# Kernel optimization log

Measured on AMD Instinct MI355X. Metric: run time of the kernel, lower is better.

## Reference

```python
import jax, jax.numpy as jnp
from jax import lax
import numpy as np

B, CB, HW, HID, P, NC = 128, 200, 32, 32, 4, 10
DEPTH, D, DI, DS, DR, K = 4, 128, 256, 16, 8, 4
G = HW // P                  # 8 -> 64 spatial patches
SPA_N = G * G
SPE_N = CB // 2              # 100 spectral patches
HS, HE = HW // 2 - 5 // 2, HW // 2 + 5 // 2 + 1   # centered 5x5 spectral crop: 14:19


def _sincos_1d(d, pos):
    omega = 1.0 / 10000 ** (np.arange(d // 2, dtype=np.float64) / (d / 2.0))
    out = np.outer(pos.reshape(-1).astype(np.float64), omega)
    return np.concatenate([np.sin(out), np.cos(out)], axis=1)


def _spa_pos_embed():
    # MAE get_2d_sincos_pos_embed with cls_token=True (zeros row FIRST)
    gw, gh = np.meshgrid(np.arange(G, dtype=np.float64), np.arange(G, dtype=np.float64))
    emb = np.concatenate([_sincos_1d(D // 2, gw), _sincos_1d(D // 2, gh)], axis=1)
    return np.concatenate([np.zeros((1, D)), emb], axis=0)  # (SPA_N+1, D)


def _spe_pos_embed():
    pe = np.zeros((SPE_N + 1, D))
    pos = np.arange(SPE_N + 1, dtype=np.float64)[:, None]
    div = np.exp(np.arange(0, D, 2) * -(np.log(10000.0) / D))
    pe[:, 0::2] = np.sin(pos * div)
    pe[:, 1::2] = np.cos(pos * div)
    return pe


def setup_inputs():
    keys = iter(jax.random.split(jax.random.key(0), 64))
    r = lambda shape, s=0.02: jax.random.normal(next(keys), shape, jnp.float32) * s
    return dict(
        x=jax.random.normal(next(keys), (B, CB, HW, HW), jnp.float32),
        spa_pos=jnp.asarray(_spa_pos_embed(), jnp.float32),
        spe_pos=jnp.asarray(_spe_pos_embed(), jnp.float32),
        dr_w1=r((HID, CB)), dr_b1=r((HID,)), bn1_g=1.0 + r((HID,)), bn1_b=r((HID,)),
        dr_w2=r((HID, HID)), dr_b2=r((HID,)), bn2_g=1.0 + r((HID,)), bn2_b=r((HID,)),
        spa_pw=r((D, HID, P, P)), spa_pb=r((D,)),
        spe_pw=r((D, 25, 2)), spe_pb=r((D,)),
        spa_cls=r((1, 1, D)), spe_cls=r((1, 1, D)),
        ln_g=jnp.ones((DEPTH, 2, D), jnp.float32), ln_b=jnp.zeros((DEPTH, 2, D), jnp.float32),
        in_w=r((DEPTH, 2, 2 * DI, D)),
        conv_w=r((DEPTH, 2, DI, K), 0.2), conv_b=r((DEPTH, 2, DI)),
        xp_w=r((DEPTH, 2, DR + 2 * DS, DI)),
        dtp_w=r((DEPTH, 2, DI, DR), 0.1), dtp_b=r((DEPTH, 2, DI), 0.1),
        a_log=jnp.log(jnp.tile(jnp.arange(1.0, DS + 1.0, dtype=jnp.float32), (DEPTH, 2, DI, 1))),
        d_p=jnp.ones((DEPTH, 2, DI), jnp.float32),
        out_w=r((DEPTH, 2, D, DI)),
        l1_w=r((DEPTH, D, D)),
        head_w=r((NC, D)), head_b=r((NC,)),
    )


def _layernorm(x, g, b, eps=1e-6):
    m = x.mean(-1, keepdims=True)
    v = jnp.mean((x - m) ** 2, axis=-1, keepdims=True)
    return (x - m) * lax.rsqrt(v + eps) * g + b


def _batchnorm(x, g, b, eps=1e-5):
    # training-mode BN: biased batch stats over (B,H,W) per channel
    m = x.mean((0, 2, 3), keepdims=True)
    v = x.var((0, 2, 3), keepdims=True)
    return (x - m) * lax.rsqrt(v + eps) * g[None, :, None, None] + b[None, :, None, None]


def _ssm(x, in_w, cw, cb, xpw, dtw, dtb, alog, dpar, ow):
    # standard Mamba selective-scan block (expand=2, d_conv=4)
    Bb, L, _ = x.shape
    xz = jnp.einsum('bld,ed->ble', x, in_w)
    xc, z = jnp.split(xz, 2, axis=-1)
    xt = jnp.pad(xc.transpose(0, 2, 1), ((0, 0), (0, 0), (K - 1, 0)))  # causal pad
    xt = lax.conv_general_dilated(xt, cw[:, None, :], (1,), 'VALID', feature_group_count=DI)
    xc = jax.nn.silu(xt + cb[None, :, None]).transpose(0, 2, 1)        # (B,L,DI)
    dbl = jnp.einsum('bld,ed->ble', xc, xpw)
    dt = jax.nn.softplus(jnp.einsum('blr,dr->bld', dbl[..., :DR], dtw) + dtb)
    Bm, Cm = dbl[..., DR:DR + DS], dbl[..., DR + DS:]
    dA = jnp.exp(dt[..., None] * (-jnp.exp(alog)))                     # (B,L,DI,DS)
    dBx = (dt * xc)[..., None] * Bm[:, :, None, :]                     # (B,L,DI,DS)

    def step(h, ab):
        h = ab[0] * h + ab[1]
        return h, h

    _, hs = lax.scan(step, jnp.zeros((Bb, DI, DS), xc.dtype),
                     (dA.transpose(1, 0, 2, 3), dBx.transpose(1, 0, 2, 3)))
    y = jnp.einsum('lbds,bls->bld', hs, Cm) + xc * dpar
    return jnp.einsum('bld,ed->ble', y * jax.nn.silu(z), ow)


def _block(inp, lg, lb, sp):
    # block_1D: bidirectional SSM with trailing cls token kept in place
    xn = _layernorm(inp, lg, lb)
    x1 = _ssm(xn, *sp)
    x2 = jnp.concatenate([xn[:, :-1][:, ::-1], xn[:, -1:]], axis=1)
    x3 = _ssm(x2, *sp)
    x3 = jnp.concatenate([x3[:, :-1][:, ::-1], x3[:, -1:]], axis=1)
    return (x1 + x3) * 0.5 + inp


def reference(x, spa_pos, spe_pos, dr_w1, dr_b1, bn1_g, bn1_b, dr_w2, dr_b2, bn2_g, bn2_b,
              spa_pw, spa_pb, spe_pw, spe_pb, spa_cls, spe_cls, ln_g, ln_b, in_w, conv_w,
              conv_b, xp_w, dtp_w, dtp_b, a_log, d_p, out_w, l1_w, head_w, head_b):
    Bb = x.shape[0]
    # dimen_redu: 1x1 conv -> BN -> ReLU -> 1x1 conv -> BN
    h = jnp.einsum('bchw,oc->bohw', x, dr_w1) + dr_b1[None, :, None, None]
    h = jax.nn.relu(_batchnorm(h, bn1_g, bn1_b))
    h = jnp.einsum('bchw,oc->bohw', h, dr_w2) + dr_b2[None, :, None, None]
    h = _batchnorm(h, bn2_g, bn2_b)
    # spatial patch embed (conv k=stride=P == patchify + matmul)
    hr = h.reshape(Bb, HID, G, P, G, P)
    x_spa = jnp.einsum('bcipjq,dcpq->bijd', hr, spa_pw).reshape(Bb, SPA_N, D) + spa_pb
    x_spa = x_spa + spa_pos[None, :-1, :]
    x_spa = jnp.concatenate([x_spa, jnp.broadcast_to(spa_cls + spa_pos[None, -1:, :], (Bb, 1, D))], axis=1)
    # spectral patch embed on centered 5x5 crop: Conv1d(25->D, k=stride=2) over bands
    xc = x[:, :, HS:HE, HS:HE].reshape(Bb, CB, 25).transpose(0, 2, 1).reshape(Bb, 25, SPE_N, 2)
    x_spe = jnp.einsum('bcls,dcs->bld', xc, spe_pw) + spe_pb
    x_spe = x_spe + spe_pos[None, :-1, :]
    x_spe = jnp.concatenate([x_spe, jnp.broadcast_to(spe_cls + spe_pos[None, -1:, :], (Bb, 1, D))], axis=1)
    for i in range(DEPTH):
        spa_p = (in_w[i, 0], conv_w[i, 0], conv_b[i, 0], xp_w[i, 0], dtp_w[i, 0], dtp_b[i, 0], a_log[i, 0], d_p[i, 0], out_w[i, 0])
        spe_p = (in_w[i, 1], conv_w[i, 1], conv_b[i, 1], xp_w[i, 1], dtp_w[i, 1], dtp_b[i, 1], a_log[i, 1], d_p[i, 1], out_w[i, 1])
        x_spa = _block(x_spa, ln_g[i, 0], ln_b[i, 0], spa_p)
        x_spe = _block(x_spe, ln_g[i, 1], ln_b[i, 1], spe_p)
        # sigmoid-gated fusion (fu=True)
        c = (x_spa[:, (x_spa.shape[1] - 1) // 2, :] + x_spe.mean(axis=1)) * 0.5
        sig = jax.nn.sigmoid(c @ l1_w[i].T)[:, None, :]
        x_spa = x_spa * sig
        x_spe = x_spe * sig
    out = (x_spa[:, -1] + x_spe[:, -1]) * 0.5   # cls tokens (global_pool=False)
    return out @ head_w.T + head_b
```

## Files before the change

### kernel.cpp

```cpp
#include <hip/hip_runtime.h>
#include <math.h>

typedef float4 f4;
typedef __attribute__((ext_vector_type(8))) short short8v;
typedef __attribute__((ext_vector_type(4))) float f32x4;

constexpr int B_ = 128, CB_ = 200, HW_ = 32, HID_ = 32, D_ = 128, DI_ = 256;
constexpr int DS_ = 16, DR_ = 8, KC_ = 4, DEPTH_ = 4, NC_ = 10;
constexpr int LSPA_ = 65, LSPE_ = 101, NPIX_ = 1024;
constexpr int M1_ = B_ * NPIX_;
constexpr int NSPA4 = B_*LSPA_*D_/4;
constexpr int NSPE4 = B_*LSPE_*D_/4;
constexpr int NW_ = DEPTH_*2*512*D_;

constexpr size_t O_XSPA = 0;
constexpr size_t O_XSPE = O_XSPA + (size_t)B_*LSPA_*D_;
constexpr size_t O_SC   = O_XSPE + (size_t)B_*LSPE_*D_;
constexpr size_t O_BN1P = O_SC + 512;
constexpr size_t O_BN2P = O_BN1P + 512*64;
constexpr size_t O_U    = O_BN2P + 512*64;
constexpr size_t O_HP1  = O_U;
constexpr size_t O_HP2  = O_U + (size_t)M1_*HID_;
constexpr size_t O_WTR  = O_HP2 + (size_t)M1_*HID_;
constexpr size_t O_XZSPA = O_U;
constexpr size_t O_XZSPE = O_XZSPA + (size_t)B_*LSPA_*512;
constexpr size_t O_XCSPA = O_XZSPE + (size_t)B_*LSPE_*512;
constexpr size_t O_XCSPE = O_XCSPA + (size_t)2*B_*LSPA_*DI_;
constexpr size_t O_DBSPA = O_XCSPE + (size_t)2*B_*LSPE_*DI_;
constexpr size_t O_DBSPE = O_DBSPA + (size_t)2*B_*LSPA_*40;
constexpr size_t O_YZSPA = O_DBSPE + (size_t)2*B_*LSPE_*40;
constexpr size_t O_YZSPE = O_YZSPA + (size_t)2*B_*LSPA_*DI_;
constexpr size_t O_WHI  = O_YZSPE + (size_t)2*B_*LSPE_*DI_;
constexpr size_t O_WLO  = O_WHI + NW_/2;

static __device__ __forceinline__ unsigned short f2bf(float f) {
    unsigned int u = __float_as_uint(f);
    unsigned int r = u + 0x7fffu + ((u >> 16) & 1u);
    return (unsigned short)(r >> 16);
}
static __device__ __forceinline__ float bf2f(unsigned short h) {
    return __uint_as_float(((unsigned int)h) << 16);
}

__global__ __launch_bounds__(256) void k_stem1(const float* __restrict__ x,
        const float* __restrict__ w1, const float* __restrict__ b1,
        float* __restrict__ hpre1, float* __restrict__ part)
{
    __shared__ float smem[8448];
    float* sw = smem;
    const int t = threadIdx.x;
    for (int i = t; i < CB_*HID_; i += 256) {
        int c = i >> 5, o = i & 31;
        sw[i] = w1[o*CB_ + c];
    }
    const int m = blockIdx.x*256 + t;
    const int b = m >> 10, pix = m & 1023;
    const float* xp = x + (size_t)b*CB_*NPIX_ + pix;
    float h[HID_];
    #pragma unroll
    for (int o = 0; o < HID_; o++) h[o] = b1[o];
    __syncthreads();
    for (int c8 = 0; c8 < CB_; c8 += 8) {
        float xv[8];
        #pragma unroll
        for (int j = 0; j < 8; j++) xv[j] = xp[(size_t)(c8 + j)*NPIX_];
        #pragma unroll
        for (int j = 0; j < 8; j++) {
            const f4* wr = (const f4*)(sw + (c8 + j)*HID_);
            #pragma unroll
            for (int o8 = 0; o8 < 8; o8++) {
                f4 wv = wr[o8];
                h[o8*4+0] = fmaf(xv[j], wv.x, h[o8*4+0]);
                h[o8*4+1] = fmaf(xv[j], wv.y, h[o8*4+1]);
                h[o8*4+2] = fmaf(xv[j], wv.z, h[o8*4+2]);
                h[o8*4+3] = fmaf(xv[j], wv.w, h[o8*4+3]);
            }
        }
    }
    f4* hp = (f4*)(hpre1 + (size_t)m*HID_);
    #pragma unroll
    for (int o = 0; o < HID_; o += 4) { f4 v = {h[o],h[o+1],h[o+2],h[o+3]}; hp[o>>2] = v; }
    __syncthreads();
    float* sred = smem;
    #pragma unroll
    for (int o = 0; o < HID_; o++) sred[t*33 + o] = h[o];
    __syncthreads();
    if (t < HID_) {
        float s = 0.f, q = 0.f;
        for (int j = 0; j < 256; j++) { float v = sred[j*33 + t]; s += v; q += v*v; }
        part[blockIdx.x*64 + t]      = s;
        part[blockIdx.x*64 + 32 + t] = q;
    }
}

__global__ void k_bnfix(const float* __restrict__ part, const float* __restrict__ g,
        const float* __restrict__ bta, float* __restrict__ scale, float* __restrict__ shift)
{
    const int o = threadIdx.x;
    if (o >= 32) return;
    float s = 0.f, q = 0.f;
    for (int j = 0; j < 512; j++) { s += part[j*64 + o]; q += part[j*64 + 32 + o]; }
    const float mean = s / (float)M1_;
    const float var  = q / (float)M1_ - mean*mean;
    const float sc = g[o] * rsqrtf(var + 1e-5f);
    scale[o] = sc;
    shift[o] = bta[o] - mean*sc;
}

__global__ void k_bnfix_spa(const float* __restrict__ part, const float* __restrict__ g,
        const float* __restrict__ bta, const float* __restrict__ spa_pw,
        const float* __restrict__ spa_pb, float* __restrict__ scale,
        float* __restrict__ shift, float* __restrict__ spa_shift)
{
    __shared__ float ssh[32];
    const int t = threadIdx.x;
    if (t < 32) {
// ... 1 lines not shown
        for (int j = 0; j < 512; j++) { s += part[j*64 + t]; q += part[j*64 + 32 + t]; }
        const float mean = s / (float)M1_;
        const float var  = q / (float)M1_ - mean*mean;
        const float sc = g[t] * rsqrtf(var + 1e-5f);
        scale[t] = sc;
        const float sh = bta[t] - mean*sc;
        shift[t] = sh;
        ssh[t] = sh;
    }
    __syncthreads();
    float acc = spa_pb[t];
    for (int c = 0; c < HID_; c++) {
        float wsum = 0.f;
        #pragma unroll
        for (int pq = 0; pq < 16; pq++) wsum += spa_pw[((size_t)t*HID_ + c)*16 + pq];
        acc = fmaf(ssh[c], wsum, acc);
    }
    spa_shift[t] = acc;
}

__global__ __launch_bounds__(256) void k_stem2(const float* __restrict__ hpre1,
        const float* __restrict__ w2, const float* __restrict__ b2,
        const float* __restrict__ sc1, const float* __restrict__ sh1,
        float* __restrict__ hpre2, float* __restrict__ part)
{
    __shared__ float smem[8448];
    __shared__ float s_sc[HID_], s_sh[HID_], s_b2[HID_];
    float* sw = smem;
    const int t = threadIdx.x;
    for (int i = t; i < HID_*HID_; i += 256) {
        int c = i >> 5, o = i & 31;
        sw[i] = w2[o*HID_ + c];
    }
    if (t < HID_) { s_sc[t] = sc1[t]; s_sh[t] = sh1[t]; s_b2[t] = b2[t]; }
    __syncthreads();
    const int m = blockIdx.x*256 + t;
    const f4* hp = (const f4*)(hpre1 + (size_t)m*HID_);
    float a[HID_];
    #pragma unroll
    for (int c = 0; c < HID_; c += 4) { f4 v = hp[c>>2]; a[c]=v.x; a[c+1]=v.y; a[c+2]=v.z; a[c+3]=v.w; }
    #pragma unroll
    for (int c = 0; c < HID_; c++) a[c] = fmaxf(fmaf(a[c], s_sc[c], s_sh[c]), 0.f);
    float h[HID_];
    #pragma unroll
    for (int o = 0; o < HID_; o++) h[o] = s_b2[o];
    #pragma unroll
    for (int c = 0; c < HID_; c++) {
        const f4* wr = (const f4*)(sw + c*HID_);
        #pragma unroll
        for (int o8 = 0; o8 < 8; o8++) {
            f4 wv = wr[o8];
            h[o8*4+0] = fmaf(a[c], wv.x, h[o8*4+0]);
            h[o8*4+1] = fmaf(a[c], wv.y, h[o8*4+1]);
            h[o8*4+2] = fmaf(a[c], wv.z, h[o8*4+2]);
            h[o8*4+3] = fmaf(a[c], wv.w, h[o8*4+3]);
        }
    }
    f4* op = (f4*)(hpre2 + (size_t)m*HID_);
    #pragma unroll
    for (int o = 0; o < HID_; o += 4) { f4 v = {h[o],h[o+1],h[o+2],h[o+3]}; op[o>>2] = v; }
    __syncthreads();
    float* sred = smem;
    #pragma unroll
    for (int o = 0; o < HID_; o++) sred[t*33 + o] = h[o];
    __syncthreads();
    if (t < HID_) {
        float s = 0.f, q = 0.f;
        for (int j = 0; j < 256; j++) { float v = sred[j*33 + t]; s += v; q += v*v; }
        part[blockIdx.x*64 + t]      = s;
        part[blockIdx.x*64 + 32 + t] = q;
    }
}

__global__ __launch_bounds__(256) void k_wtr(const float* __restrict__ spa_pw,
        float* __restrict__ wtr)
{
    const int idx = blockIdx.x*256 + threadIdx.x;
    if (idx >= 65536) return;
    const int pq = idx >> 12, dc = idx & 4095;
    wtr[idx] = spa_pw[dc*16 + pq];
}

__global__ __launch_bounds__(256) void k_wsplit(const float* __restrict__ in_w,
        unsigned short* __restrict__ whi, unsigned short* __restrict__ wlo)
{
    const int i = blockIdx.x*256 + threadIdx.x;
    if (i >= NW_) return;
    const float f = in_w[i];
    const unsigned short h = f2bf(f);
    whi[i] = h;
    wlo[i] = f2bf(f - bf2f(h));
}

__global__ __launch_bounds__(256) void k_patch(const float* __restrict__ hpre2,
        const float* __restrict__ wtr, const float* __restrict__ sc2,
        const float* __restrict__ spa_shift, const float* __restrict__ spa_pos,
        const float* __restrict__ spa_cls, float* __restrict__ xspa)
{
    const int b = blockIdx.x >> 1, half = blockIdx.x & 1;
    const int n0 = half*32;
    __shared__ __align__(16) float sA[32*36];
    __shared__ __align__(16) float sB[128*36];
    __shared__ float s_sc[HID_];
    const int t = threadIdx.x;
    if (t < HID_) s_sc[t] = sc2[t];
    const int ty = t >> 4, tx = t & 15;
    float acc[2][8];
    #pragma unroll
    for (int i = 0; i < 2; i++)
        #pragma unroll
        for (int j = 0; j < 8; j++) acc[i][j] = 0.f;
    for (int pq = 0; pq < 16; pq++) {
        const int p = pq >> 2, q = pq & 3;
        __syncthreads();
        for (int idx = t; idx < 32*8; idx += 256) {
            const int n = idx >> 3, c4 = (idx & 7)*4;
            const int nn = n0 + n;
            const int ii = nn >> 3, jj = nn & 7;
            const int pix = (ii*4 + p)*HW_ + jj*4 + q;
            f4 v = *(const f4*)(hpre2 + ((size_t)b*NPIX_ + pix)*HID_ + c4);
            float* pp = &sA[n*36 + c4];
            pp[0] = v.x*s_sc[c4]; pp[1] = v.y*s_sc[c4+1]; pp[2] = v.z*s_sc[c4+2]; pp[3] = v.w*s_sc[c4+3];
        }
        for (int idx = t; idx < 128*8; idx += 256) {
            const int dd = idx >> 3, c4 = (idx & 7)*4;
            f4 v = *(const f4*)(wtr + pq*4096 + dd*HID_ + c4);
            float* pp = &sB[dd*36 + c4];
            pp[0]=v.x; pp[1]=v.y; pp[2]=v.z; pp[3]=v.w;
        }
        __syncthreads();
        #pragma unroll
        for (int kq = 0; kq < 8; kq++) {
            f4 a0 = *(const f4*)&sA[(ty*2+0)*36 + kq*4];
            f4 a1 = *(const f4*)&sA[(ty*2+1)*36 + kq*4];
            #pragma unroll
            for (int j = 0; j < 8; j++) {
                const f4 bv = *(const f4*)&sB[(tx + 16*j)*36 + kq*4];
                acc[0][j] = fmaf(a0.x,bv.x,fmaf(a0.y,bv.y,fmaf(a0.z,bv.z,fmaf(a0.w,bv.w,acc[0][j]))));
                acc[1][j] = fmaf(a1.x,bv.x,fmaf(a1.y,bv.y,fmaf(a1.z,bv.z,fmaf(a1.w,bv.w,acc[1][j]))));
            }
        }
    }
    #pragma unroll
    for (int i = 0; i < 2; i++) {
        const int n = n0 + ty*2 + i;
        float* orow = xspa + ((size_t)b*LSPA_ + n)*D_;
        #pragma unroll
        for (int j = 0; j < 8; j++) {
            const int d = tx + 16*j;
            orow[d] = acc[i][j] + spa_shift[d] + spa_pos[n*D_ + d];
        }
    }
    if (half == 0 && t < D_)
        xspa[((size_t)b*LSPA_ + 64)*D_ + t] = spa_cls[t] + spa_pos[64*D_ + t];
}

__global__ __launch_bounds__(256) void k_spe(const float* __restrict__ x,
        const float* __restrict__ spe_pw, const float* __restrict__ spe_pb,
        const float* __restrict__ spe_pos, const float* __restrict__ spe_cls,
        float* __restrict__ xspe)
{
    const int b = blockIdx.x >> 1, half = blockIdx.x & 1;
    __shared__ float sx[100*25];
    __shared__ float sw[D_*51];
    const int t = threadIdx.x;
    for (int idx = t; idx < 100*25; idx += 256) {
        const int ch = idx / 25 + half*100, c = idx % 25;
        sx[idx] = x[(size_t)b*CB_*NPIX_ + (size_t)ch*NPIX_ + (14 + c/5)*HW_ + 14 + c%5];
    }
    for (int idx = t; idx < D_*50; idx += 256) sw[(idx/50)*51 + idx%50] = spe_pw[idx];
    __syncthreads();
    const int d = t & 127, ls = t >> 7;
    for (int j = ls; j < 50; j += 2) {
        const int l = half*50 + j;
// ... 97 lines not shown
            dh[0] = h0; dh[1] = h1;
            dl[0] = l0; dl[1] = l1;
        }
        __syncthreads();
        short8v ah[2], al[2], bh[4], bl[4];
        #pragma unroll
        for (int i = 0; i < 2; i++) {
            const int ro = (wm*32 + i*16 + lr)*136 + kc*32 + lg*8;
            ah[i] = *(const short8v*)&sAhi[ro];
            al[i] = *(const short8v*)&sAlo[ro];
        }
        #pragma unroll
        for (int j = 0; j < 4; j++) {
            const int co = (wn*64 + j*16 + lr)*40 + lg*8;
            bh[j] = *(const short8v*)&sBhi[co];
            bl[j] = *(const short8v*)&sBlo[co];
        }
        #pragma unroll
        for (int i = 0; i < 2; i++)
            #pragma unroll
            for (int j = 0; j < 4; j++) {
                acc[i][j] = __builtin_amdgcn_mfma_f32_16x16x32_bf16(ah[i], bh[j], acc[i][j], 0, 0, 0);
                acc[i][j] = __builtin_amdgcn_mfma_f32_16x16x32_bf16(ah[i], bl[j], acc[i][j], 0, 0, 0);
                acc[i][j] = __builtin_amdgcn_mfma_f32_16x16x32_bf16(al[i], bh[j], acc[i][j], 0, 0, 0);
            }
        __syncthreads();
    }

    #pragma unroll
    for (int i = 0; i < 2; i++) {
        const int rbase = m0 + wm*32 + i*16 + lg*4;
        #pragma unroll
        for (int j = 0; j < 4; j++) {
            const int col = n0 + wn*64 + j*16 + lr;
            #pragma unroll
            for (int r = 0; r < 4; r++)
                XZ[(size_t)(rbase + r)*512 + col] = acc[i][j][r];
        }
    }
}

__global__ __launch_bounds__(256) void k_conv(const float* __restrict__ xz_spa,
        const float* __restrict__ xz_spe, float* __restrict__ xc_spa, float* __restrict__ xc_spe,
        const float* __restrict__ conv_w, const float* __restrict__ conv_b, int depth)
{
    const int br = blockIdx.z;
    const int L = br ? LSPE_ : LSPA_;
    const int nt = (L + 15) / 16;
    const int b = blockIdx.x % B_;
    const int tl = blockIdx.x / B_;
    if (tl >= nt) return;
    const int l0 = tl * 16;
    const int d = threadIdx.x;
    const float* XZ = (br ? xz_spe : xz_spa) + (size_t)b*L*512 + d;
    float* XC0 = (br ? xc_spe : xc_spa) + ((size_t)(0*B_ + b)*L)*DI_ + d;
    float* XC1 = (br ? xc_spe : xc_spa) + ((size_t)(1*B_ + b)*L)*DI_ + d;
    const size_t w = (size_t)depth*2 + br;
    const float* cw = conv_w + (w*DI_ + d)*KC_;
    const float cb = conv_b[w*DI_ + d];
    const float w0 = cw[0], w1 = cw[1], w2 = cw[2], w3 = cw[3];
    float av[19], ev[19];
    #pragma unroll
    for (int j = 0; j < 19; j++) {
        const int l = l0 - 3 + j;
        const bool ok = (l >= 0) && (l < L);
        av[j] = ok ? XZ[(size_t)l*512] : 0.f;
        const int lr = (l == L-1) ? (L-1) : (L-2-l);
        ev[j] = ok ? XZ[(size_t)lr*512] : 0.f;
    }
    #pragma unroll
    for (int c = 0; c < 16; c++) {
        const int l = l0 + c;
        if (l < L) {
            float acc0 = fmaf(av[c],w0, fmaf(av[c+1],w1, fmaf(av[c+2],w2, fmaf(av[c+3],w3, cb))));
            float acc1 = fmaf(ev[c],w0, fmaf(ev[c+1],w1, fmaf(ev[c+2],w2, fmaf(ev[c+3],w3, cb))));
            XC0[(size_t)l*DI_] = acc0 / (1.f + __expf(-acc0));
            XC1[(size_t)l*DI_] = acc1 / (1.f + __expf(-acc1));
        }
    }
}

__global__ __launch_bounds__(256) void k_xp(const float* __restrict__ xc_spa,
        const float* __restrict__ xc_spe, float* __restrict__ dbl_spa, float* __restrict__ dbl_spe,
        const float* __restrict__ xp_w, int depth)
{
    const int br = blockIdx.z;
    const int L = br ? LSPE_ : LSPA_;
    const int M2 = 2*B_*L;
    const int tile = blockIdx.x;
    if (tile*64 >= M2) return;
    const float* XC = br ? xc_spe : xc_spa;
    float* DBL = br ? dbl_spe : dbl_spa;
    const float* W = xp_w + ((size_t)depth*2 + br)*40*DI_;
    __shared__ __align__(16) float sA[64*68];
    __shared__ __align__(16) float sB[40*68];
    const int t = threadIdx.x;
    const int m0 = tile*64;
    const int ty = t >> 2, tx = t & 3;
    float acc[10];
    #pragma unroll
    for (int j = 0; j < 10; j++) acc[j] = 0.f;
    for (int kc = 0; kc < 4; kc++) {
        __syncthreads();
        for (int idx = t; idx < 64*16; idx += 256) {
            const int r = idx >> 4, k4 = (idx & 15)*4;
            f4 v = *(const f4*)(XC + ((size_t)(m0 + r))*DI_ + kc*64 + k4);
            float* p = &sA[r*68 + k4];
            p[0]=v.x; p[1]=v.y; p[2]=v.z; p[3]=v.w;
        }
        for (int idx = t; idx < 40*16; idx += 256) {
            const int n = idx >> 4, k4 = (idx & 15)*4;
            f4 v = *(const f4*)(W + (size_t)n*DI_ + kc*64 + k4);
            float* p = &sB[n*68 + k4];
            p[0]=v.x; p[1]=v.y; p[2]=v.z; p[3]=v.w;
        }
        __syncthreads();
        #pragma unroll
        for (int kq = 0; kq < 16; kq++) {
            const f4 a = *(const f4*)&sA[ty*68 + kq*4];
            #pragma unroll
            for (int j = 0; j < 10; j++) {
                const f4 bv = *(const f4*)&sB[(tx*10 + j)*68 + kq*4];
                acc[j] = fmaf(a.x,bv.x,fmaf(a.y,bv.y,fmaf(a.z,bv.z,fmaf(a.w,bv.w,acc[j]))));
            }
        }
    }
    float* outp = DBL + (size_t)(m0 + ty)*40 + tx*10;
    #pragma unroll
    for (int j = 0; j < 10; j++) outp[j] = acc[j];
}

__global__ __launch_bounds__(256) void k_scan(
        const float* __restrict__ xz_spa, const float* __restrict__ xz_spe,
        const float* __restrict__ xc_spa, const float* __restrict__ xc_spe,
        const float* __restrict__ dbl_spa, const float* __restrict__ dbl_spe,
        float* __restrict__ yz_spa, float* __restrict__ yz_spe,
        const float* __restrict__ a_log, const float* __restrict__ dtp_w,
        const float* __restrict__ dtp_b, const float* __restrict__ d_p, int depth)
{
    const int br = blockIdx.z, dir = blockIdx.y;
    const int L = br ? LSPE_ : LSPA_;
    const int b = blockIdx.x;
    const int t = threadIdx.x;
    const float* XZ   = (br ? xz_spe : xz_spa) + (size_t)b*L*512;
    const float* XC   = (br ? xc_spe : xc_spa) + ((size_t)(dir*B_ + b))*L*DI_;
    const float* DBLp = (br ? dbl_spe : dbl_spa) + ((size_t)(dir*B_ + b))*L*40;
    float* YZ = (br ? yz_spe : yz_spa) + ((size_t)(dir*B_ + b))*L*DI_;
    const size_t w = (size_t)depth*2 + br;
    const float nA0 = -__expf(a_log[((size_t)(w*DI_ + t))*DS_]) * 1.4426950408889634f;
    float dtw[8];
    #pragma unroll
    for (int r = 0; r < 8; r++) dtw[r] = dtp_w[((size_t)(w*DI_ + t))*DR_ + r];
    const float dtb = dtp_b[w*DI_ + t];
    const float dpv = d_p[w*DI_ + t];
    float h[16];
    #pragma unroll
    for (int u = 0; u < 16; u++) h[u] = 0.f;

    __shared__ __align__(16) float sD[2][320];
    float rd0, rd1;
    float rxA[8], rzA[8], rxB[8], rzB[8];

#define LOADD(J0) do {                                                        \
    const int lim_ = ((L - (J0) < 8) ? (L - (J0)) : 8) * 40;                  \
    rd0 = (t < lim_) ? DBLp[(size_t)(J0)*40 + t] : 0.f;                       \
    rd1 = (t + 256 < lim_) ? DBLp[(size_t)(J0)*40 + t + 256] : 0.f;           \
} while(0)

#define WRITED(BUF) do {                                                      \
    sD[BUF][t] = rd0;                                                         \
    if (t < 64) sD[BUF][t + 256] = rd1;                                       \
} while(0)

#define LOADX(J0, RX, RZ) do {                                                \
    _Pragma("unroll")                                                         \
    for (int j_ = 0; j_ < 8; ++j_) {                                          \
        const int row_ = (J0) + j_;                                           \
        if (row_ < L) {                                                       \
            RX[j_] = XC[(size_t)row_*DI_ + t];                                \
            const int zr_ = dir ? ((row_ == L-1) ? (L-1) : (L-2-row_)) : row_;\
            RZ[j_] = XZ[(size_t)zr_*512 + 256 + t];                           \
        } else { RX[j_] = 0.f; RZ[j_] = 0.f; }                                \
    }                                                                         \
} while(0)

#define SCAN_CHUNK(J0, BUF, RX, RZ) do {                                      \
    _Pragma("unroll")                                                         \
    for (int c_ = 0; c_ < 8; ++c_) {                                          \
        const int l_ = (J0) + c_;                                             \
        if (l_ < L) {                                                         \
            const float* dr = &sD[BUF][c_*40];                                \
            const f4 q0 = *(const f4*)(dr);                                   \
            const f4 q1 = *(const f4*)(dr + 4);                               \
            float raw = dtb;                                                  \
            raw = fmaf(q0.x,dtw[0],raw); raw = fmaf(q0.y,dtw[1],raw);         \
            raw = fmaf(q0.z,dtw[2],raw); raw = fmaf(q0.w,dtw[3],raw);         \
            raw = fmaf(q1.x,dtw[4],raw); raw = fmaf(q1.y,dtw[5],raw);         \
            raw = fmaf(q1.z,dtw[6],raw); raw = fmaf(q1.w,dtw[7],raw);         \
            const float er = __builtin_amdgcn_exp2f(raw * 1.4426950408889634f);\
            const float dt = (raw > 20.f) ? raw                               \
                : __log2f(1.f + er) * 0.6931471805599453f;                    \
            const float xcv = RX[c_], zv = RZ[c_];                            \
            const float c2 = dt * xcv;                                        \
            const float E1 = __builtin_amdgcn_exp2f(nA0 * dt);                \
            const float E2 = E1 * E1;                                         \
            const f4 B0=*(const f4*)(dr+8),  B1=*(const f4*)(dr+12);          \
            const f4 B2=*(const f4*)(dr+16), B3=*(const f4*)(dr+20);          \
            const f4 C0=*(const f4*)(dr+24), C1=*(const f4*)(dr+28);          \
            const f4 C2=*(const f4*)(dr+32), C3=*(const f4*)(dr+36);          \
            float eo = E1, ee = E2, y = 0.f;                                  \
            h[0]=fmaf(h[0],eo,c2*B0.x);  y=fmaf(h[0],C0.x,y);                 \
            h[1]=fmaf(h[1],ee,c2*B0.y);  y=fmaf(h[1],C0.y,y);                 \
            eo*=E2; h[2]=fmaf(h[2],eo,c2*B0.z);  y=fmaf(h[2],C0.z,y);         \
            ee*=E2; h[3]=fmaf(h[3],ee,c2*B0.w);  y=fmaf(h[3],C0.w,y);         \
            eo*=E2; h[4]=fmaf(h[4],eo,c2*B1.x);  y=fmaf(h[4],C1.x,y);         \
            ee*=E2; h[5]=fmaf(h[5],ee,c2*B1.y);  y=fmaf(h[5],C1.y,y);         \
            eo*=E2; h[6]=fmaf(h[6],eo,c2*B1.z);  y=fmaf(h[6],C1.z,y);         \
            ee*=E2; h[7]=fmaf(h[7],ee,c2*B1.w);  y=fmaf(h[7],C1.w,y);         \
            eo*=E2; h[8]=fmaf(h[8],eo,c2*B2.x);  y=fmaf(h[8],C2.x,y);         \
            ee*=E2; h[9]=fmaf(h[9],ee,c2*B2.y);  y=fmaf(h[9],C2.y,y);         \
            eo*=E2; h[10]=fmaf(h[10],eo,c2*B2.z); y=fmaf(h[10],C2.z,y);       \
            ee*=E2; h[11]=fmaf(h[11],ee,c2*B2.w); y=fmaf(h[11],C2.w,y);       \
            eo*=E2; h[12]=fmaf(h[12],eo,c2*B3.x); y=fmaf(h[12],C3.x,y);       \
            ee*=E2; h[13]=fmaf(h[13],ee,c2*B3.y); y=fmaf(h[13],C3.y,y);       \
            eo*=E2; h[14]=fmaf(h[14],eo,c2*B3.z); y=fmaf(h[14],C3.z,y);       \
            ee*=E2; h[15]=fmaf(h[15],ee,c2*B3.w); y=fmaf(h[15],C3.w,y);       \
            const float yt = fmaf(xcv, dpv, y);                               \
            const float sg = __builtin_amdgcn_rcpf(                           \
                1.f + __builtin_amdgcn_exp2f(-zv * 1.4426950408889634f));     \
            const int ls_ = dir ? ((l_ == L-1) ? (L-1) : (L-2-l_)) : l_;      \
            YZ[(size_t)ls_*DI_ + t] = yt * (zv * sg);                         \
        }                                                                     \
    }                                                                         \
} while(0)

    const int nch = (L + 7) >> 3;
    LOADD(0);
    LOADX(0, rxA, rzA);
    WRITED(0);
    __syncthreads();
    int ck = 0;
    while (true) {
        {
            const int j0 = ck*8;
            const bool more = (ck + 1 < nch);
            if (more) { LOADD(j0 + 8); LOADX(j0 + 8, rxB, rzB); }
            SCAN_CHUNK(j0, 0, rxA, rzA);
            if (more) WRITED(1);
            __syncthreads();
            if (!more) break;
            ck++;
        }
        {
            const int j0 = ck*8;
            const bool more = (ck + 1 < nch);
            if (more) { LOADD(j0 + 8); LOADX(j0 + 8, rxA, rzA); }
            SCAN_CHUNK(j0, 1, rxB, rzB);
            if (more) WRITED(0);
            __syncthreads();
            if (!more) break;
            ck++;
        }
    }
#undef LOADD
#undef WRITED
#undef LOADX
#undef SCAN_CHUNK
}

__global__ __launch_bounds__(256) void k_out(float* __restrict__ xspa, float* __restrict__ xspe,
        const float* __restrict__ yz_spa, const float* __restrict__ yz_spe,
        const float* __restrict__ out_w, int depth)
{
    const int br = blockIdx.z;
    const int L = br ? LSPE_ : LSPA_;
    const int M = B_ * L;
    const int tile = blockIdx.x;
    if (tile*32 >= M) return;
    float* X = br ? xspe : xspa;
    const float* Y0 = br ? yz_spe : yz_spa;
    const float* Y1 = Y0 + (size_t)B_*L*DI_;
    const float* W = out_w + ((size_t)depth*2 + br)*D_*DI_;
    __shared__ __align__(16) float sA[32*68];
    __shared__ __align__(16) float sB[128*68];
    const int t = threadIdx.x;
    const int m0 = tile*32;
    const int ty = t >> 4, tx = t & 15;
    float acc[2][8];
    #pragma unroll
    for (int i = 0; i < 2; i++)
        #pragma unroll
        for (int j = 0; j < 8; j++) acc[i][j] = 0.f;
    for (int kc = 0; kc < 4; kc++) {
        __syncthreads();
        for (int idx = t; idx < 32*16; idx += 256) {
            const int r = idx >> 4, k4 = (idx & 15)*4;
            const size_t go = ((size_t)(m0 + r))*DI_ + kc*64 + k4;
            f4 v0 = *(const f4*)(Y0 + go);
            f4 v1 = *(const f4*)(Y1 + go);
            float* p = &sA[r*68 + k4];
            p[0]=v0.x+v1.x; p[1]=v0.y+v1.y; p[2]=v0.z+v1.z; p[3]=v0.w+v1.w;
        }
        for (int idx = t; idx < 128*64; idx += 256) {
            const int n = idx >> 6, kk = idx & 63;
            sB[n*68 + kk] = W[(size_t)n*DI_ + kc*64 + kk];
        }
        __syncthreads();
        #pragma unroll
        for (int kq = 0; kq < 16; kq++) {
            f4 a0 = *(const f4*)&sA[(ty*2+0)*68 + kq*4];
            f4 a1 = *(const f4*)&sA[(ty*2+1)*68 + kq*4];
            #pragma unroll
            for (int j = 0; j < 8; j++) {
                const f4 bv = *(const f4*)&sB[(tx + 16*j)*68 + kq*4];
                acc[0][j] = fmaf(a0.x,bv.x,fmaf(a0.y,bv.y,fmaf(a0.z,bv.z,fmaf(a0.w,bv.w,acc[0][j]))));
                acc[1][j] = fmaf(a1.x,bv.x,fmaf(a1.y,bv.y,fmaf(a1.z,bv.z,fmaf(a1.w,bv.w,acc[1][j]))));
            }
        }
    }
    #pragma unroll
    for (int i = 0; i < 2; i++) {
        float* orow = X + (size_t)(m0 + ty*2 + i)*D_;
        #pragma unroll
        for (int j = 0; j < 8; j++) {
            const int n = tx + 16*j;
            orow[n] += 0.5f*acc[i][j];
        }
    }
}

__global__ __launch_bounds__(256) void k_gate1(const float* __restrict__ xspa,
        const float* __restrict__ xspe, const float* __restrict__ l1_w,
        float* __restrict__ sig, int depth)
{
    __shared__ float sp[2][128];
    __shared__ float sc[128];
    __shared__ float sduo[256];
    const int b = blockIdx.x, t = threadIdx.x;
    const int dd = t & 127, rh = t >> 7;
    float s = 0.f;
    for (int l = rh; l < LSPE_; l += 2) s += xspe[((size_t)b*LSPE_ + l)*D_ + dd];
    sp[rh][dd] = s;
    __syncthreads();
    if (t < 128)
        sc[t] = 0.5f*(xspa[((size_t)b*LSPA_ + 32)*D_ + t] + (sp[0][t]+sp[1][t])*(1.f/101.f));
    __syncthreads();
    {
        const float* wr = l1_w + (size_t)depth*D_*D_ + (size_t)dd*D_ + rh*64;
        float acc = 0.f;
        #pragma unroll 4
        for (int k = 0; k < 64; k++) acc = fmaf(sc[rh*64 + k], wr[k], acc);
        sduo[t] = acc;
    }
    __syncthreads();
    if (t < 128)
        sig[(size_t)b*D_ + t] = 1.f/(1.f + __expf(-(sduo[t] + sduo[t+128])));
}

__global__ __launch_bounds__(256) void k_gate2(float* __restrict__ xspa,
        float* __restrict__ xspe, const float* __restrict__ sig)
{
    const int fi = blockIdx.x*256 + threadIdx.x;
    f4* base;
    int b, pos;
    if (fi < NSPA4) {
        base = (f4*)xspa + fi;
        b = fi / (LSPA_*32);
        pos = fi & 31;
    } else {
        const int j = fi - NSPA4;
        if (j >= NSPE4) return;
        base = (f4*)xspe + j;
        b = j / (LSPE_*32);
        pos = j & 31;
    }
    const f4 sg = *((const f4*)sig + b*32 + pos);
    f4 v = *base;
    v.x *= sg.x; v.y *= sg.y; v.z *= sg.z; v.w *= sg.w;
    *base = v;
}

__global__ void k_head(const float* __restrict__ xspa, const float* __restrict__ xspe,
        const float* __restrict__ head_w, const float* __restrict__ head_b, float* __restrict__ out)
{
    __shared__ float sv[D_];
    const int b = blockIdx.x, t = threadIdx.x;
    if (t < D_) sv[t] = 0.5f*(xspa[((size_t)b*LSPA_ + 64)*D_ + t] + xspe[((size_t)b*LSPE_ + 100)*D_ + t]);
    __syncthreads();
    if (t < NC_) {
        float acc = head_b[t];
        for (int k = 0; k < D_; k++) acc = fmaf(sv[k], head_w[t*D_ + k], acc);
        out[b*NC_ + t] = acc;
    }
}

extern "C" void kernel_launch(void* const* d_in, const int* in_sizes, int n_in,
                              void* d_out, int out_size, void* d_ws, size_t ws_size,
                              hipStream_t stream)
{
    const float* x       = (const float*)d_in[0];
    const float* spa_pos = (const float*)d_in[1];
    const float* spe_pos = (const float*)d_in[2];
    const float* dr_w1   = (const float*)d_in[3];
    const float* dr_b1   = (const float*)d_in[4];
    const float* bn1_g   = (const float*)d_in[5];
    const float* bn1_b   = (const float*)d_in[6];
    const float* dr_w2   = (const float*)d_in[7];
    const float* dr_b2   = (const float*)d_in[8];
    const float* bn2_g   = (const float*)d_in[9];
    const float* bn2_b   = (const float*)d_in[10];
    const float* spa_pw  = (const float*)d_in[11];
    const float* spa_pb  = (const float*)d_in[12];
    const float* spe_pw  = (const float*)d_in[13];
    const float* spe_pb  = (const float*)d_in[14];
    const float* spa_cls = (const float*)d_in[15];
    const float* spe_cls = (const float*)d_in[16];
    const float* ln_g    = (const float*)d_in[17];
    const float* ln_b    = (const float*)d_in[18];
    const float* in_w    = (const float*)d_in[19];
    const float* conv_w  = (const float*)d_in[20];
    const float* conv_b  = (const float*)d_in[21];
    const float* xp_w    = (const float*)d_in[22];
    const float* dtp_w   = (const float*)d_in[23];
    const float* dtp_b   = (const float*)d_in[24];
    const float* a_log   = (const float*)d_in[25];
    const float* d_p     = (const float*)d_in[26];
    const float* out_w   = (const float*)d_in[27];
    const float* l1_w    = (const float*)d_in[28];
    const float* head_w  = (const float*)d_in[29];
    const float* head_b  = (const float*)d_in[30];

    float* ws = (float*)d_ws;
    float* xspa   = ws + O_XSPA;
    float* xspe   = ws + O_XSPE;
    float* scale1 = ws + O_SC;
    float* shift1 = ws + O_SC + 32;
    float* scale2 = ws + O_SC + 64;
    float* shift2 = ws + O_SC + 96;
    float* spa_sh = ws + O_SC + 128;
    float* bn1p   = ws + O_BN1P;
    float* bn2p   = ws + O_BN2P;
    float* sig    = ws + O_BN1P;
    float* hpre1  = ws + O_HP1;
    float* hpre2  = ws + O_HP2;
    float* wtr    = ws + O_WTR;
    float* xz_spa = ws + O_XZSPA;
    float* xz_spe = ws + O_XZSPE;
    float* xc_spa = ws + O_XCSPA;
    float* xc_spe = ws + O_XCSPE;
    float* db_spa = ws + O_DBSPA;
    float* db_spe = ws + O_DBSPE;
    float* yz_spa = ws + O_YZSPA;
    float* yz_spe = ws + O_YZSPE;
    unsigned short* whi = (unsigned short*)(ws + O_WHI);
    unsigned short* wlo = (unsigned short*)(ws + O_WLO);

    hipLaunchKernelGGL(k_stem1, dim3(512), dim3(256), 0, stream, x, dr_w1, dr_b1, hpre1, bn1p);
    hipLaunchKernelGGL(k_bnfix, dim3(1), dim3(32), 0, stream, bn1p, bn1_g, bn1_b, scale1, shift1);
    hipLaunchKernelGGL(k_wtr, dim3(256), dim3(256), 0, stream, spa_pw, wtr);
    hipLaunchKernelGGL(k_wsplit, dim3(NW_/256), dim3(256), 0, stream, in_w, whi, wlo);
    hipLaunchKernelGGL(k_stem2, dim3(512), dim3(256), 0, stream, hpre1, dr_w2, dr_b2, scale1, shift1, hpre2, bn2p);
    hipLaunchKernelGGL(k_bnfix_spa, dim3(1), dim3(128), 0, stream, bn2p, bn2_g, bn2_b,
                       spa_pw, spa_pb, scale2, shift2, spa_sh);
    hipLaunchKernelGGL(k_patch, dim3(256), dim3(256), 0, stream, hpre2, wtr, scale2, spa_sh, spa_pos, spa_cls, xspa);
    hipLaunchKernelGGL(k_spe, dim3(256), dim3(256), 0, stream, x, spe_pw, spe_pb, spe_pos, spe_cls, xspe);

    for (int i = 0; i < DEPTH_; i++) {
        hipLaunchKernelGGL(k_ln_in, dim3(202, 4, 2), dim3(256), 0, stream,
                           xspa, xspe, xz_spa, xz_spe, whi, wlo, ln_g, ln_b, i);
        hipLaunchKernelGGL(k_conv, dim3(B_*7, 1, 2), dim3(256), 0, stream,
                           xz_spa, xz_spe, xc_spa, xc_spe, conv_w, conv_b, i);
        hipLaunchKernelGGL(k_xp, dim3(404, 1, 2), dim3(256), 0, stream,
                           xc_spa, xc_spe, db_spa, db_spe, xp_w, i);
        hipLaunchKernelGGL(k_scan, dim3(B_, 2, 2), dim3(256), 0, stream,
                           xz_spa, xz_spe, xc_spa, xc_spe, db_spa, db_spe,
                           yz_spa, yz_spe, a_log, dtp_w, dtp_b, d_p, i);
        hipLaunchKernelGGL(k_out, dim3(404, 1, 2), dim3(256), 0, stream,
                           xspa, xspe, yz_spa, yz_spe, out_w, i);
        hipLaunchKernelGGL(k_gate1, dim3(128), dim3(256), 0, stream, xspa, xspe, l1_w, sig, i);
        hipLaunchKernelGGL(k_gate2, dim3((NSPA4 + NSPE4 + 255)/256), dim3(256), 0, stream,
                           xspa, xspe, sig);
    }
    hipLaunchKernelGGL(k_head, dim3(128), dim3(128), 0, stream,
                       xspa, xspe, head_w, head_b, (float*)d_out);
}
```

Before: 868.4 us.

## Port x_proj and out_proj GEMMs to split-bf16 MFMA with pre-split weights

Rewrites the x_proj and out_proj GEMM kernels to use bf16 MFMA 16x16x32 instructions instead of scalar FP32 FMAs. Each operand is split into a bf16 high part and a bf16 residual, and three MFMAs per tile pair keep near-FP32 accuracy. Weights are pre-split once in the extended k_wsplit kernel, while activations are split on the fly as they are staged into shared memory. Tile sizes double, which halves the grid. The cost is extra conversion work, more shared memory, and wasted MFMA columns, since x_proj's 40 output columns are padded to 48.

```diff
diff --git a/kernel.cpp b/kernel.cpp
--- a/kernel.cpp
+++ b/kernel.cpp
@@ -11,7 +11,9 @@
 constexpr int M1_ = B_ * NPIX_;
 constexpr int NSPA4 = B_*LSPA_*D_/4;
 constexpr int NSPE4 = B_*LSPE_*D_/4;
-constexpr int NW_ = DEPTH_*2*512*D_;
+constexpr int NWI_ = DEPTH_*2*512*D_;
+constexpr int NWO_ = DEPTH_*2*D_*DI_;
+constexpr int NWX_ = DEPTH_*2*40*DI_;
 
 constexpr size_t O_XSPA = 0;
 constexpr size_t O_XSPE = O_XSPA + (size_t)B_*LSPA_*D_;
@@ -30,8 +32,12 @@
 constexpr size_t O_DBSPE = O_DBSPA + (size_t)2*B_*LSPA_*40;
 constexpr size_t O_YZSPA = O_DBSPE + (size_t)2*B_*LSPE_*40;
 constexpr size_t O_YZSPE = O_YZSPA + (size_t)2*B_*LSPA_*DI_;
-constexpr size_t O_WHI  = O_YZSPE + (size_t)2*B_*LSPE_*DI_;
-constexpr size_t O_WLO  = O_WHI + NW_/2;
+constexpr size_t O_WHI_I = O_YZSPE + (size_t)2*B_*LSPE_*DI_;
+constexpr size_t O_WLO_I = O_WHI_I + NWI_/2;
+constexpr size_t O_WHI_O = O_WLO_I + NWI_/2;
+constexpr size_t O_WLO_O = O_WHI_O + NWO_/2;
+constexpr size_t O_WHI_X = O_WLO_O + NWO_/2;
+constexpr size_t O_WLO_X = O_WHI_X + NWX_/2;
 
 static __device__ __forceinline__ unsigned short f2bf(float f) {
     unsigned int u = __float_as_uint(f);
@@ -199,14 +205,20 @@
 }
 
 __global__ __launch_bounds__(256) void k_wsplit(const float* __restrict__ in_w,
-        unsigned short* __restrict__ whi, unsigned short* __restrict__ wlo)
+        const float* __restrict__ out_w, const float* __restrict__ xp_w,
+        unsigned short* __restrict__ whiI, unsigned short* __restrict__ wloI,
+        unsigned short* __restrict__ whiO, unsigned short* __restrict__ wloO,
+        unsigned short* __restrict__ whiX, unsigned short* __restrict__ wloX)
 {
     const int i = blockIdx.x*256 + threadIdx.x;
-    if (i >= NW_) return;
-    const float f = in_w[i];
+    float f; unsigned short* ph; unsigned short* pl; int j;
+    if (i < NWI_) { j = i; f = in_w[j]; ph = whiI; pl = wloI; }
+    else if (i < NWI_ + NWO_) { j = i - NWI_; f = out_w[j]; ph = whiO; pl = wloO; }
+    else if (i < NWI_ + NWO_ + NWX_) { j = i - NWI_ - NWO_; f = xp_w[j]; ph = whiX; pl = wloX; }
+    else return;
     const unsigned short h = f2bf(f);
-    whi[i] = h;
-    wlo[i] = f2bf(f - bf2f(h));
+    ph[j] = h;
+    pl[j] = f2bf(f - bf2f(h));
 }
 
 __global__ __launch_bounds__(256) void k_patch(const float* __restrict__ hpre2,
@@ -470,52 +482,106 @@
 
 __global__ __launch_bounds__(256) void k_xp(const float* __restrict__ xc_spa,
         const float* __restrict__ xc_spe, float* __restrict__ dbl_spa, float* __restrict__ dbl_spe,
-        const float* __restrict__ xp_w, int depth)
+        const unsigned short* __restrict__ whiX, const unsigned short* __restrict__ wloX, int depth)
 {
     const int br = blockIdx.z;
     const int L = br ? LSPE_ : LSPA_;
     const int M2 = 2*B_*L;
-    const int tile = blockIdx.x;
-    if (tile*64 >= M2) return;
+    const int m0 = blockIdx.x*128;
+    if (m0 >= M2) return;
     const float* XC = br ? xc_spe : xc_spa;
     float* DBL = br ? dbl_spe : dbl_spa;
-    const float* W = xp_w + ((size_t)depth*2 + br)*40*DI_;
-    __shared__ __align__(16) float sA[64*68];
-    __shared__ __align__(16) float sB[40*68];
+    const size_t wb = ((size_t)depth*2 + br) * 40 * (size_t)DI_;
+    const unsigned short* WH = whiX + wb;
+    const unsigned short* WL = wloX + wb;
+
+    __shared__ __align__(16) unsigned short sAhi[128*40];
+    __shared__ __align__(16) unsigned short sAlo[128*40];
+    __shared__ __align__(16) unsigned short sBhi[48*40];
+    __shared__ __align__(16) unsigned short sBlo[48*40];
+
     const int t = threadIdx.x;
-    const int m0 = tile*64;
-    const int ty = t >> 2, tx = t & 3;
-    float acc[10];
-    #pragma unroll
-    for (int j = 0; j < 10; j++) acc[j] = 0.f;
-    for (int kc = 0; kc < 4; kc++) {
+    const int wv = t >> 6, l = t & 63;
+    const int lr = l & 15, lg = l >> 4;
+    f32x4 acc[2][3];
+    #pragma unroll
+    for (int i = 0; i < 2; i++)
+        #pragma unroll
+        for (int j = 0; j < 3; j++) acc[i][j] = (f32x4){0.f,0.f,0.f,0.f};
+
+    for (int kc = 0; kc < 8; kc++) {
+        {
+            const int r = t >> 1, off = (t & 1)*16;
+            const float* src = XC + (size_t)(m0 + r)*DI_ + kc*32 + off;
+            unsigned short uh[16], ul[16];
+            #pragma unroll
+            for (int j4 = 0; j4 < 4; j4++) {
+                f4 u = *(const f4*)(src + j4*4);
+                float vv[4] = {u.x, u.y, u.z, u.w};
+                #pragma unroll
+                for (int e = 0; e < 4; e++) {
+                    const unsigned short h = f2bf(vv[e]);
+                    uh[j4*4+e] = h;
+                    ul[j4*4+e] = f2bf(vv[e] - bf2f(h));
+                }
+            }
+            #pragma unroll
+            for (int j4 = 0; j4 < 4; j4++) {
+                ushort4 a = {uh[j4*4], uh[j4*4+1], uh[j4*4+2], uh[j4*4+3]};
+                ushort4 b = {ul[j4*4], ul[j4*4+1], ul[j4*4+2], ul[j4*4+3]};
+                *(ushort4*)&sAhi[r*40 + off + j4*4] = a;
+                *(ushort4*)&sAlo[r*40 + off + j4*4] = b;
+            }
+            if (t < 192) {
+                const int n = t >> 2, q = t & 3;
+                uint4 h0 = {0,0,0,0}, l0 = {0,0,0,0};
+                if (n < 40) {
+                    const size_t g = (size_t)n*DI_ + kc*32 + q*8;
+                    h0 = *(const uint4*)(WH + g);
+                    l0 = *(const uint4*)(WL + g);
+                }
+                *(uint4*)&sBhi[n*40 + q*8] = h0;
+                *(uint4*)&sBlo[n*40 + q*8] = l0;
+            }
+        }
         __syncthreads();
-        for (int idx = t; idx < 64*16; idx += 256) {
-            const int r = idx >> 4, k4 = (idx & 15)*4;
-            f4 v = *(const f4*)(XC + ((size_t)(m0 + r))*DI_ + kc*64 + k4);
-            float* p = &sA[r*68 + k4];
-            p[0]=v.x; p[1]=v.y; p[2]=v.z; p[3]=v.w;
-        }
-        for (int idx = t; idx < 40*16; idx += 256) {
-            const int n = idx >> 4, k4 = (idx & 15)*4;
-            f4 v = *(const f4*)(W + (size_t)n*DI_ + kc*64 + k4);
-            float* p = &sB[n*68 + k4];
-            p[0]=v.x; p[1]=v.y; p[2]=v.z; p[3]=v.w;
-        }
+        short8v ah[2], al[2], bh[3], bl[3];
+        #pragma unroll
+        for (int i = 0; i < 2; i++) {
+            const int ro = (wv*32 + i*16 + lr)*40 + lg*8;
+            ah[i] = *(const short8v*)&sAhi[ro];
+            al[i] = *(const short8v*)&sAlo[ro];
+        }
+        #pragma unroll
+        for (int j = 0; j < 3; j++) {
+            const int co = (j*16 + lr)*40 + lg*8;
+            bh[j] = *(const short8v*)&sBhi[co];
+            bl[j] = *(const short8v*)&sBlo[co];
+        }
+        #pragma unroll
+        for (int i = 0; i < 2; i++)
+            #pragma unroll
+            for (int j = 0; j < 3; j++) {
+                acc[i][j] = __builtin_amdgcn_mfma_f32_16x16x32_bf16(ah[i], bh[j], acc[i][j], 0, 0, 0);
+                acc[i][j] = __builtin_amdgcn_mfma_f32_16x16x32_bf16(ah[i], bl[j], acc[i][j], 0, 0, 0);
+                acc[i][j] = __builtin_amdgcn_mfma_f32_16x16x32_bf16(al[i], bh[j], acc[i][j], 0, 0, 0);
+            }
         __syncthreads();
-        #pragma unroll
-        for (int kq = 0; kq < 16; kq++) {
-            const f4 a = *(const f4*)&sA[ty*68 + kq*4];
-            #pragma unroll
-            for (int j = 0; j < 10; j++) {
-                const f4 bv = *(const f4*)&sB[(tx*10 + j)*68 + kq*4];
-                acc[j] = fmaf(a.x,bv.x,fmaf(a.y,bv.y,fmaf(a.z,bv.z,fmaf(a.w,bv.w,acc[j]))));
-            }
-        }
-    }
-    float* outp = DBL + (size_t)(m0 + ty)*40 + tx*10;
-    #pragma unroll
-    for (int j = 0; j < 10; j++) outp[j] = acc[j];
+    }
+
+    #pragma unroll
+    for (int i = 0; i < 2; i++) {
+        const int rbase = m0 + wv*32 + i*16 + lg*4;
+        #pragma unroll
+        for (int j = 0; j < 3; j++) {
+            const int col = j*16 + lr;
+            if (col < 40) {
+                #pragma unroll
+                for (int r = 0; r < 4; r++)
+                    DBL[(size_t)(rbase + r)*40 + col] = acc[i][j][r];
+            }
+        }
+    }
 }
 
 __global__ __launch_bounds__(256) void k_scan(
@@ -658,61 +724,104 @@
 
 __global__ __launch_bounds__(256) void k_out(float* __restrict__ xspa, float* __restrict__ xspe,
         const float* __restrict__ yz_spa, const float* __restrict__ yz_spe,
-        const float* __restrict__ out_w, int depth)
+        const unsigned short* __restrict__ whiO, const unsigned short* __restrict__ wloO, int depth)
 {
     const int br = blockIdx.z;
     const int L = br ? LSPE_ : LSPA_;
     const int M = B_ * L;
-    const int tile = blockIdx.x;
-    if (tile*32 >= M) return;
+    const int m0 = blockIdx.x*64;
+    if (m0 >= M) return;
     float* X = br ? xspe : xspa;
     const float* Y0 = br ? yz_spe : yz_spa;
     const float* Y1 = Y0 + (size_t)B_*L*DI_;
-    const float* W = out_w + ((size_t)depth*2 + br)*D_*DI_;
-    __shared__ __align__(16) float sA[32*68];
-    __shared__ __align__(16) float sB[128*68];
+    const size_t wb = ((size_t)depth*2 + br) * (size_t)D_ * DI_;
+    const unsigned short* WH = whiO + wb;
+    const unsigned short* WL = wloO + wb;
+
+    __shared__ __align__(16) unsigned short sAhi[64*40];
+    __shared__ __align__(16) unsigned short sAlo[64*40];
+    __shared__ __align__(16) unsigned short sBhi[128*40];
+    __shared__ __align__(16) unsigned short sBlo[128*40];
+
     const int t = threadIdx.x;
-    const int m0 = tile*32;
-    const int ty = t >> 4, tx = t & 15;
-    float acc[2][8];
+    const int wv = t >> 6, l = t & 63;
+    const int wm = wv >> 1, wn = wv & 1;
+    const int lr = l & 15, lg = l >> 4;
+    f32x4 acc[2][4];
     #pragma unroll
     for (int i = 0; i < 2; i++)
         #pragma unroll
-        for (int j = 0; j < 8; j++) acc[i][j] = 0.f;
-    for (int kc = 0; kc < 4; kc++) {
+        for (int j = 0; j < 4; j++) acc[i][j] = (f32x4){0.f,0.f,0.f,0.f};
+
+    for (int kc = 0; kc < 8; kc++) {
+        {
+            const int r = t >> 2, q = t & 3;
+            const size_t g = (size_t)(m0 + r)*DI_ + kc*32 + q*8;
+            unsigned short uh[8], ul[8];
+            #pragma unroll
+            for (int j4 = 0; j4 < 2; j4++) {
+                f4 u0 = *(const f4*)(Y0 + g + j4*4);
+                f4 u1 = *(const f4*)(Y1 + g + j4*4);
+                float vv[4] = {u0.x+u1.x, u0.y+u1.y, u0.z+u1.z, u0.w+u1.w};
+                #pragma unroll
+                for (int e = 0; e < 4; e++) {
+                    const unsigned short hh = f2bf(vv[e]);
+                    uh[j4*4+e] = hh;
+                    ul[j4*4+e] = f2bf(vv[e] - bf2f(hh));
+                }
+            }
+            #pragma unroll
+            for (int j4 = 0; j4 < 2; j4++) {
+                ushort4 a = {uh[j4*4], uh[j4*4+1], uh[j4*4+2], uh[j4*4+3]};
+                ushort4 b = {ul[j4*4], ul[j4*4+1], ul[j4*4+2], ul[j4*4+3]};
+                *(ushort4*)&sAhi[r*40 + q*8 + j4*4] = a;
+                *(ushort4*)&sAlo[r*40 + q*8 + j4*4] = b;
+            }
+            const int n = t >> 1, off = (t & 1)*16;
+            const size_t gb = (size_t)n*DI_ + kc*32 + off;
+            uint4 h0 = *(const uint4*)(WH + gb);
+            uint4 h1 = *(const uint4*)(WH + gb + 8);
+            uint4 l0 = *(const uint4*)(WL + gb);
+            uint4 l1 = *(const uint4*)(WL + gb + 8);
+            uint4* dh = (uint4*)&sBhi[n*40 + off];
+            uint4* dl = (uint4*)&sBlo[n*40 + off];
+            dh[0] = h0; dh[1] = h1;
+            dl[0] = l0; dl[1] = l1;
+        }
         __syncthreads();
-        for (int idx = t; idx < 32*16; idx += 256) {
-            const int r = idx >> 4, k4 = (idx & 15)*4;
-            const size_t go = ((size_t)(m0 + r))*DI_ + kc*64 + k4;
-            f4 v0 = *(const f4*)(Y0 + go);
-            f4 v1 = *(const f4*)(Y1 + go);
-            float* p = &sA[r*68 + k4];
-            p[0]=v0.x+v1.x; p[1]=v0.y+v1.y; p[2]=v0.z+v1.z; p[3]=v0.w+v1.w;
-        }
-        for (int idx = t; idx < 128*64; idx += 256) {
-            const int n = idx >> 6, kk = idx & 63;
-            sB[n*68 + kk] = W[(size_t)n*DI_ + kc*64 + kk];
-        }
+        short8v ah[2], al[2], bh[4], bl[4];
+        #pragma unroll
+        for (int i = 0; i < 2; i++) {
+            const int ro = (wm*32 + i*16 + lr)*40 + lg*8;
+            ah[i] = *(const short8v*)&sAhi[ro];
+            al[i] = *(const short8v*)&sAlo[ro];
+        }
+        #pragma unroll
+        for (int j = 0; j < 4; j++) {
+            const int co = (wn*64 + j*16 + lr)*40 + lg*8;
+            bh[j] = *(const short8v*)&sBhi[co];
+            bl[j] = *(const short8v*)&sBlo[co];
+        }
+        #pragma unroll
+        for (int i = 0; i < 2; i++)
+            #pragma unroll
+            for (int j = 0; j < 4; j++) {
+                acc[i][j] = __builtin_amdgcn_mfma_f32_16x16x32_bf16(ah[i], bh[j], acc[i][j], 0, 0, 0);
+                acc[i][j] = __builtin_amdgcn_mfma_f32_16x16x32_bf16(ah[i], bl[j], acc[i][j], 0, 0, 0);
+                acc[i][j] = __builtin_amdgcn_mfma_f32_16x16x32_bf16(al[i], bh[j], acc[i][j], 0, 0, 0);
+            }
         __syncthreads();
-        #pragma unroll
-        for (int kq = 0; kq < 16; kq++) {
-            f4 a0 = *(const f4*)&sA[(ty*2+0)*68 + kq*4];
-            f4 a1 = *(const f4*)&sA[(ty*2+1)*68 + kq*4];
-            #pragma unroll
-            for (int j = 0; j < 8; j++) {
-                const f4 bv = *(const f4*)&sB[(tx + 16*j)*68 + kq*4];
-                acc[0][j] = fmaf(a0.x,bv.x,fmaf(a0.y,bv.y,fmaf(a0.z,bv.z,fmaf(a0.w,bv.w,acc[0][j]))));
-                acc[1][j] = fmaf(a1.x,bv.x,fmaf(a1.y,bv.y,fmaf(a1.z,bv.z,fmaf(a1.w,bv.w,acc[1][j]))));
-            }
-        }
-    }
+    }
+
     #pragma unroll
     for (int i = 0; i < 2; i++) {
-        float* orow = X + (size_t)(m0 + ty*2 + i)*D_;
-        #pragma unroll
-        for (int j = 0; j < 8; j++) {
-            const int n = tx + 16*j;
-            orow[n] += 0.5f*acc[i][j];
+        const int rbase = m0 + wm*32 + i*16 + lg*4;
+        #pragma unroll
+        for (int j = 0; j < 4; j++) {
+            const int col = wn*64 + j*16 + lr;
+            #pragma unroll
+            for (int r = 0; r < 4; r++)
+                X[(size_t)(rbase + r)*D_ + col] += 0.5f*acc[i][j][r];
         }
     }
 }
@@ -840,13 +949,18 @@
     float* db_spe = ws + O_DBSPE;
     float* yz_spa = ws + O_YZSPA;
     float* yz_spe = ws + O_YZSPE;
-    unsigned short* whi = (unsigned short*)(ws + O_WHI);
-    unsigned short* wlo = (unsigned short*)(ws + O_WLO);
+    unsigned short* whiI = (unsigned short*)(ws + O_WHI_I);
+    unsigned short* wloI = (unsigned short*)(ws + O_WLO_I);
+    unsigned short* whiO = (unsigned short*)(ws + O_WHI_O);
+    unsigned short* wloO = (unsigned short*)(ws + O_WLO_O);
+    unsigned short* whiX = (unsigned short*)(ws + O_WHI_X);
+    unsigned short* wloX = (unsigned short*)(ws + O_WLO_X);
 
     hipLaunchKernelGGL(k_stem1, dim3(512), dim3(256), 0, stream, x, dr_w1, dr_b1, hpre1, bn1p);
     hipLaunchKernelGGL(k_bnfix, dim3(1), dim3(32), 0, stream, bn1p, bn1_g, bn1_b, scale1, shift1);
     hipLaunchKernelGGL(k_wtr, dim3(256), dim3(256), 0, stream, spa_pw, wtr);
-    hipLaunchKernelGGL(k_wsplit, dim3(NW_/256), dim3(256), 0, stream, in_w, whi, wlo);
+    hipLaunchKernelGGL(k_wsplit, dim3((NWI_+NWO_+NWX_+255)/256), dim3(256), 0, stream,
+                       in_w, out_w, xp_w, whiI, wloI, whiO, wloO, whiX, wloX);
     hipLaunchKernelGGL(k_stem2, dim3(512), dim3(256), 0, stream, hpre1, dr_w2, dr_b2, scale1, shift1, hpre2, bn2p);
     hipLaunchKernelGGL(k_bnfix_spa, dim3(1), dim3(128), 0, stream, bn2p, bn2_g, bn2_b,
                        spa_pw, spa_pb, scale2, shift2, spa_sh);
@@ -855,16 +969,16 @@
 
     for (int i = 0; i < DEPTH_; i++) {
         hipLaunchKernelGGL(k_ln_in, dim3(202, 4, 2), dim3(256), 0, stream,
-                           xspa, xspe, xz_spa, xz_spe, whi, wlo, ln_g, ln_b, i);
+                           xspa, xspe, xz_spa, xz_spe, whiI, wloI, ln_g, ln_b, i);
         hipLaunchKernelGGL(k_conv, dim3(B_*7, 1, 2), dim3(256), 0, stream,
                            xz_spa, xz_spe, xc_spa, xc_spe, conv_w, conv_b, i);
-        hipLaunchKernelGGL(k_xp, dim3(404, 1, 2), dim3(256), 0, stream,
-                           xc_spa, xc_spe, db_spa, db_spe, xp_w, i);
+        hipLaunchKernelGGL(k_xp, dim3(202, 1, 2), dim3(256), 0, stream,
+                           xc_spa, xc_spe, db_spa, db_spe, whiX, wloX, i);
         hipLaunchKernelGGL(k_scan, dim3(B_, 2, 2), dim3(256), 0, stream,
                            xz_spa, xz_spe, xc_spa, xc_spe, db_spa, db_spe,
                            yz_spa, yz_spe, a_log, dtp_w, dtp_b, d_p, i);
-        hipLaunchKernelGGL(k_out, dim3(404, 1, 2), dim3(256), 0, stream,
-                           xspa, xspe, yz_spa, yz_spe, out_w, i);
+        hipLaunchKernelGGL(k_out, dim3(202, 1, 2), dim3(256), 0, stream,
+                           xspa, xspe, yz_spa, yz_spe, whiO, wloO, i);
         hipLaunchKernelGGL(k_gate1, dim3(128), dim3(256), 0, stream, xspa, xspe, l1_w, sig, i);
         hipLaunchKernelGGL(k_gate2, dim3((NSPA4 + NSPE4 + 255)/256), dim3(256), 0, stream,
                            xspa, xspe, sig);
```

Measured after the change: 722.1 us. 16.9% less time.
